# Kernel tuning notes

Measured on AMD Instinct MI355X. Metric: run time of the kernel, lower is better.

The kernel has to match this reference:

```python
import jax, jax.numpy as jnp
import numpy as np


def setup_inputs() -> dict:
    key = jax.random.key(0)
    k1, k2, k3 = jax.random.split(key, 3)
    N, E, D = 10000, 160000, 512
    x = jax.random.normal(k1, (N, D), dtype=jnp.float32)
    edge_index = jax.random.randint(k2, (2, E), 0, N, dtype=jnp.int64)
    W = jax.random.normal(k3, (D, D), dtype=jnp.float32) * (1.0 / np.sqrt(D))
    b = jnp.zeros((D,), dtype=jnp.float32)
    return {"x": x, "edge_index": edge_index, "W": W, "b": b}


def reference(x, edge_index, W, b):
    # PyG GCNConv: add self-loops, symmetric deg^-1/2 normalization,
    # linear transform (no bias in lin), scatter-add aggregate, then + bias.
    N = x.shape[0]
    loop = jnp.arange(N, dtype=edge_index.dtype)
    src = jnp.concatenate([edge_index[0], loop])  # message sources (j)
    dst = jnp.concatenate([edge_index[1], loop])  # message targets (i)
    deg = jax.ops.segment_sum(jnp.ones(src.shape, dtype=x.dtype), dst, num_segments=N)
    deg_inv_sqrt = jnp.where(deg > 0, jax.lax.rsqrt(deg), 0.0)
    norm = deg_inv_sqrt[src] * deg_inv_sqrt[dst]  # [E+N]
    h = x @ W  # [N, D] linear transform
    msg = h[src] * norm[:, None]  # gather + scale, [E+N, D]
    out = jax.ops.segment_sum(msg, dst, num_segments=N) + b
    return out
```

## Files before the change

### kernel.cpp

```cpp
#include <hip/hip_runtime.h>
#include <stdint.h>


#define D_DIM 512
#define SLOTS 64

typedef _Float16 half8 __attribute__((ext_vector_type(8)));
typedef float floatx4 __attribute__((ext_vector_type(4)));

__global__ __launch_bounds__(256) void fused_pre_kernel(const float* __restrict__ x,
                                                        const float* __restrict__ W,
                                                        const int* __restrict__ src,
                                                        const int* __restrict__ dst,
                                                        _Float16* __restrict__ Ah,
                                                        _Float16* __restrict__ Bt,
                                                        int* __restrict__ cursor,
                                                        int* __restrict__ csr,
                                                        int total8, int nxb, int E) {
    __shared__ float tile[32][33];
    int bid = blockIdx.x;
    if (bid < nxb) {
        int i = bid * 256 + threadIdx.x;
        if (i < total8) {
            const float4* p = (const float4*)x + (size_t)i * 2;
            float4 a = p[0], bq = p[1];
            half8 h;
            h[0] = (_Float16)a.x;  h[1] = (_Float16)a.y;  h[2] = (_Float16)a.z;  h[3] = (_Float16)a.w;
            h[4] = (_Float16)bq.x; h[5] = (_Float16)bq.y; h[6] = (_Float16)bq.z; h[7] = (_Float16)bq.w;
            *((half8*)Ah + i) = h;
        }
        return;
    }
    if (bid < nxb + 256) {
        int wt = bid - nxb;
        int k0 = (wt & 15) * 32, n0 = (wt >> 4) * 32;
        int tx = threadIdx.x & 31, ty = threadIdx.x >> 5;
        #pragma unroll
        for (int r = ty; r < 32; r += 8)
            tile[r][tx] = W[(size_t)(k0 + r) * D_DIM + n0 + tx];
        __syncthreads();
        #pragma unroll
        for (int r = ty; r < 32; r += 8)
            Bt[(size_t)(n0 + r) * D_DIM + k0 + tx] = (_Float16)tile[tx][r];
        return;
    }
    int e = (bid - nxb - 256) * 256 + threadIdx.x;
    if (e < E) {
        int d = dst[e];
        int pos = atomicAdd(&cursor[d], 1);
        if (pos < SLOTS) csr[(d << 6) + pos] = src[e];
    }
}

#define GBM 128
#define GBN 128
#define GBK 32
#define LDK 40

__global__ __launch_bounds__(256) void gemm_kernel(const _Float16* __restrict__ A,
                                                   const _Float16* __restrict__ Bt,
                                                   const int* __restrict__ cursor,
                                                   _Float16* __restrict__ pre,
                                                   int M, int ngb) {
    __shared__ _Float16 Asl[2][GBM * LDK];
    __shared__ _Float16 Bsl[2][GBN * LDK];

    int tid  = threadIdx.x;
    int lane = tid & 63;
    int wave = tid >> 6;
    int wr = wave >> 1, wc = wave & 1;

    int rowbase = (blockIdx.x % ngb) * GBM;
    int colbase = (blockIdx.x / ngb) * GBN;

    int s_r = tid >> 2;
    int s_k = (tid & 3) << 3;

    int fm = lane & 15;
    int fk = (lane >> 4) << 3;

    int ar0 = rowbase + s_r;      if (ar0 >= M) ar0 = M - 1;
    int ar1 = rowbase + s_r + 64; if (ar1 >= M) ar1 = M - 1;
    const _Float16* pa0 = A  + (size_t)ar0 * D_DIM + s_k;
    const _Float16* pa1 = A  + (size_t)ar1 * D_DIM + s_k;
    const _Float16* pb0 = Bt + (size_t)(colbase + s_r) * D_DIM + s_k;
    const _Float16* pb1 = Bt + (size_t)(colbase + s_r + 64) * D_DIM + s_k;

    floatx4 acc[4][4];
    #pragma unroll
    for (int i = 0; i < 4; ++i)
        #pragma unroll
        for (int j = 0; j < 4; ++j)
            #pragma unroll
            for (int e = 0; e < 4; ++e)
                acc[i][j][e] = 0.f;

    half8 av0 = *(const half8*)pa0;
    half8 av1 = *(const half8*)pa1;
    half8 bv0 = *(const half8*)pb0;
    half8 bv1 = *(const half8*)pb1;
    *(half8*)(&Asl[0][s_r * LDK + s_k])        = av0;
    *(half8*)(&Asl[0][(s_r + 64) * LDK + s_k]) = av1;
    *(half8*)(&Bsl[0][s_r * LDK + s_k])        = bv0;
    *(half8*)(&Bsl[0][(s_r + 64) * LDK + s_k]) = bv1;

    const int KT = D_DIM / GBK;
    for (int kt = 0; kt < KT; ++kt) {
        int buf = kt & 1;
        __syncthreads();

        if (kt + 1 < KT) {
            int ko = (kt + 1) * GBK;
            av0 = *(const half8*)(pa0 + ko);
            av1 = *(const half8*)(pa1 + ko);
            bv0 = *(const half8*)(pb0 + ko);
            bv1 = *(const half8*)(pb1 + ko);
        }

        half8 afrag[4], bfrag[4];
        #pragma unroll
        for (int t = 0; t < 4; ++t) {
            afrag[t] = *(const half8*)(&Asl[buf][(wr * 64 + t * 16 + fm) * LDK + fk]);
            bfrag[t] = *(const half8*)(&Bsl[buf][(wc * 64 + t * 16 + fm) * LDK + fk]);
        }
        #pragma unroll
        for (int i = 0; i < 4; ++i)
            #pragma unroll
            for (int j = 0; j < 4; ++j)
                acc[i][j] = __builtin_amdgcn_mfma_f32_16x16x32_f16(afrag[i], bfrag[j], acc[i][j], 0, 0, 0);

        if (kt + 1 < KT) {
            int nb = buf ^ 1;
            *(half8*)(&Asl[nb][s_r * LDK + s_k])        = av0;
            *(half8*)(&Asl[nb][(s_r + 64) * LDK + s_k]) = av1;
            *(half8*)(&Bsl[nb][s_r * LDK + s_k])        = bv0;
            *(half8*)(&Bsl[nb][(s_r + 64) * LDK + s_k]) = bv1;
        }
    }

    int mrow0 = (lane >> 4) << 2;
    #pragma unroll
    for (int i = 0; i < 4; ++i) {
        #pragma unroll
        for (int r = 0; r < 4; ++r) {
            int row = rowbase + wr * 64 + i * 16 + mrow0 + r;
            if (row < M) {
                float sc = rsqrtf((float)cursor[row] + 1.0f);
                #pragma unroll
                for (int j = 0; j < 4; ++j) {
                    int col = colbase + wc * 64 + j * 16 + fm;
                    pre[(size_t)row * D_DIM + col] = (_Float16)(acc[i][j][r] * sc);
                }
            }
        }
    }
}

__global__ __launch_bounds__(256) void gather_kernel(const _Float16* __restrict__ pre,
                                                     const int* __restrict__ csr,
                                                     const int* __restrict__ cursor,
                                                     const float* __restrict__ b,
                                                     float* __restrict__ out, int N) {
    int wave = threadIdx.x >> 6;
    int lane = threadIdx.x & 63;
    int node = blockIdx.x * 4 + wave;
    if (node >= N) return;
    int c8 = lane << 3;

    int cnt = cursor[node];
    int end = cnt < SLOTS ? cnt : SLOTS;
    float di = rsqrtf((float)cnt + 1.0f);
    const int* lst = csr + (node << 6);

    float acc[8];
    {
        half8 self = *(const half8*)(pre + (size_t)node * D_DIM + c8);
        #pragma unroll
        for (int e = 0; e < 8; ++e) acc[e] = (float)self[e];
    }

    int j = 0;
    for (; j + 3 < end; j += 4) {
        int s0 = lst[j];
        int s1 = lst[j + 1];
        int s2 = lst[j + 2];
        int s3 = lst[j + 3];
        half8 v0 = *(const half8*)(pre + (size_t)s0 * D_DIM + c8);
        half8 v1 = *(const half8*)(pre + (size_t)s1 * D_DIM + c8);
        half8 v2 = *(const half8*)(pre + (size_t)s2 * D_DIM + c8);
        half8 v3 = *(const half8*)(pre + (size_t)s3 * D_DIM + c8);
        #pragma unroll
        for (int e = 0; e < 8; ++e)
            acc[e] += (float)v0[e] + (float)v1[e] + (float)v2[e] + (float)v3[e];
    }
    for (; j < end; ++j) {
        int s0 = lst[j];
        half8 v0 = *(const half8*)(pre + (size_t)s0 * D_DIM + c8);
        #pragma unroll
        for (int e = 0; e < 8; ++e) acc[e] += (float)v0[e];
    }

    float4 b0 = *(const float4*)(b + c8);
    float4 b1 = *(const float4*)(b + c8 + 4);
    floatx4 o0, o1;
    o0[0] = b0.x + di * acc[0];
    o0[1] = b0.y + di * acc[1];
    o0[2] = b0.z + di * acc[2];
    o0[3] = b0.w + di * acc[3];
    o1[0] = b1.x + di * acc[4];
    o1[1] = b1.y + di * acc[5];
    o1[2] = b1.z + di * acc[6];
    o1[3] = b1.w + di * acc[7];
    __builtin_nontemporal_store(o0, (floatx4*)(out + (size_t)node * D_DIM + c8));
    __builtin_nontemporal_store(o1, (floatx4*)(out + (size_t)node * D_DIM + c8 + 4));
}

extern "C" void kernel_launch(void* const* d_in, const int* in_sizes, int n_in,
                              void* d_out, int out_size, void* d_ws, size_t ws_size,
                              hipStream_t stream) {
    const float* x  = (const float*)d_in[0];
    const int*   ei = (const int*)d_in[1];
    const float* W  = (const float*)d_in[2];
    const float* b  = (const float*)d_in[3];
    float* out = (float*)d_out;

    int N = in_sizes[0] / D_DIM;
    int E = in_sizes[1] / 2;
    const int* src = ei;
    const int* dst = ei + E;

    char* ws = (char*)d_ws;
    size_t prebytes = (size_t)N * D_DIM * sizeof(_Float16);
    size_t ahbytes  = (size_t)N * D_DIM * sizeof(_Float16);
    size_t btbytes  = (size_t)D_DIM * D_DIM * sizeof(_Float16);
    int Npad = (N + 256) & ~255;
    _Float16* pre  = (_Float16*)ws;
    _Float16* Ah   = (_Float16*)(ws + prebytes);
    _Float16* Bt   = (_Float16*)(ws + prebytes + ahbytes);
    int*      cursor = (int*)(ws + prebytes + ahbytes + btbytes);
    int*      csr    = cursor + Npad;

    (void)hipMemsetAsync(cursor, 0, (size_t)N * sizeof(int), stream);

    int total8 = (N * D_DIM) / 8;
    int nxb = (total8 + 255) / 256;
    int degb = (E + 255) / 256;
    fused_pre_kernel<<<nxb + 256 + degb, 256, 0, stream>>>(x, W, src, dst, Ah, Bt,
                                                           cursor, csr, total8, nxb, E);

    int ngb = (N + GBM - 1) / GBM;
    gemm_kernel<<<ngb * (D_DIM / GBN), 256, 0, stream>>>(Ah, Bt, cursor, pre, N, ngb);

    gather_kernel<<<(N + 3) / 4, 256, 0, stream>>>(pre, csr, cursor, b, out, N);
}
```

Baseline: 131.0 us.

## Fuse x fp32-to-fp16 conversion into GEMM A-tile loads; unroll gather by 8

The separate pass that converted x to fp16 in the pre-kernel is removed. The GEMM now reads fp32 x directly and converts it to fp16 in registers before storing to LDS. This drops the write and re-read of a 10 MB fp16 copy of x, but each GEMM block now reads twice as many bytes per A tile and x is re-read by four column blocks. The gather kernel also gains an 8-way unrolled neighbor loop to put more loads in flight.

```diff
diff --git a/kernel.cpp b/kernel.cpp
--- a/kernel.cpp
+++ b/kernel.cpp
@@ -8,32 +8,17 @@
 typedef _Float16 half8 __attribute__((ext_vector_type(8)));
 typedef float floatx4 __attribute__((ext_vector_type(4)));
 
-__global__ __launch_bounds__(256) void fused_pre_kernel(const float* __restrict__ x,
-                                                        const float* __restrict__ W,
+__global__ __launch_bounds__(256) void fused_pre_kernel(const float* __restrict__ W,
                                                         const int* __restrict__ src,
                                                         const int* __restrict__ dst,
-                                                        _Float16* __restrict__ Ah,
                                                         _Float16* __restrict__ Bt,
                                                         int* __restrict__ cursor,
                                                         int* __restrict__ csr,
-                                                        int total8, int nxb, int E) {
+                                                        int E) {
     __shared__ float tile[32][33];
     int bid = blockIdx.x;
-    if (bid < nxb) {
-        int i = bid * 256 + threadIdx.x;
-        if (i < total8) {
-            const float4* p = (const float4*)x + (size_t)i * 2;
-            float4 a = p[0], bq = p[1];
-            half8 h;
-            h[0] = (_Float16)a.x;  h[1] = (_Float16)a.y;  h[2] = (_Float16)a.z;  h[3] = (_Float16)a.w;
-            h[4] = (_Float16)bq.x; h[5] = (_Float16)bq.y; h[6] = (_Float16)bq.z; h[7] = (_Float16)bq.w;
-            *((half8*)Ah + i) = h;
-        }
-        return;
-    }
-    if (bid < nxb + 256) {
-        int wt = bid - nxb;
-        int k0 = (wt & 15) * 32, n0 = (wt >> 4) * 32;
+    if (bid < 256) {
+        int k0 = (bid & 15) * 32, n0 = (bid >> 4) * 32;
         int tx = threadIdx.x & 31, ty = threadIdx.x >> 5;
         #pragma unroll
         for (int r = ty; r < 32; r += 8)
@@ -44,7 +29,7 @@
             Bt[(size_t)(n0 + r) * D_DIM + k0 + tx] = (_Float16)tile[tx][r];
         return;
     }
-    int e = (bid - nxb - 256) * 256 + threadIdx.x;
+    int e = (bid - 256) * 256 + threadIdx.x;
     if (e < E) {
         int d = dst[e];
         int pos = atomicAdd(&cursor[d], 1);
@@ -57,7 +42,7 @@
 #define GBK 32
 #define LDK 40
 
-__global__ __launch_bounds__(256) void gemm_kernel(const _Float16* __restrict__ A,
+__global__ __launch_bounds__(256) void gemm_kernel(const float* __restrict__ X,
                                                    const _Float16* __restrict__ Bt,
                                                    const int* __restrict__ cursor,
                                                    _Float16* __restrict__ pre,
@@ -81,8 +66,8 @@
 
     int ar0 = rowbase + s_r;      if (ar0 >= M) ar0 = M - 1;
     int ar1 = rowbase + s_r + 64; if (ar1 >= M) ar1 = M - 1;
-    const _Float16* pa0 = A  + (size_t)ar0 * D_DIM + s_k;
-    const _Float16* pa1 = A  + (size_t)ar1 * D_DIM + s_k;
+    const float* px0 = X + (size_t)ar0 * D_DIM + s_k;
+    const float* px1 = X + (size_t)ar1 * D_DIM + s_k;
     const _Float16* pb0 = Bt + (size_t)(colbase + s_r) * D_DIM + s_k;
     const _Float16* pb1 = Bt + (size_t)(colbase + s_r + 64) * D_DIM + s_k;
 
@@ -95,10 +80,15 @@
             for (int e = 0; e < 4; ++e)
                 acc[i][j][e] = 0.f;
 
-    half8 av0 = *(const half8*)pa0;
-    half8 av1 = *(const half8*)pa1;
+    float4 xa0 = *(const float4*)px0,       xb0 = *(const float4*)(px0 + 4);
+    float4 xa1 = *(const float4*)px1,       xb1 = *(const float4*)(px1 + 4);
     half8 bv0 = *(const half8*)pb0;
     half8 bv1 = *(const half8*)pb1;
+    half8 av0, av1;
+    av0[0] = (_Float16)xa0.x; av0[1] = (_Float16)xa0.y; av0[2] = (_Float16)xa0.z; av0[3] = (_Float16)xa0.w;
+    av0[4] = (_Float16)xb0.x; av0[5] = (_Float16)xb0.y; av0[6] = (_Float16)xb0.z; av0[7] = (_Float16)xb0.w;
+    av1[0] = (_Float16)xa1.x; av1[1] = (_Float16)xa1.y; av1[2] = (_Float16)xa1.z; av1[3] = (_Float16)xa1.w;
+    av1[4] = (_Float16)xb1.x; av1[5] = (_Float16)xb1.y; av1[6] = (_Float16)xb1.z; av1[7] = (_Float16)xb1.w;
     *(half8*)(&Asl[0][s_r * LDK + s_k])        = av0;
     *(half8*)(&Asl[0][(s_r + 64) * LDK + s_k]) = av1;
     *(half8*)(&Bsl[0][s_r * LDK + s_k])        = bv0;
@@ -111,8 +101,8 @@
 
         if (kt + 1 < KT) {
             int ko = (kt + 1) * GBK;
-            av0 = *(const half8*)(pa0 + ko);
-            av1 = *(const half8*)(pa1 + ko);
+            xa0 = *(const float4*)(px0 + ko); xb0 = *(const float4*)(px0 + ko + 4);
+            xa1 = *(const float4*)(px1 + ko); xb1 = *(const float4*)(px1 + ko + 4);
             bv0 = *(const half8*)(pb0 + ko);
             bv1 = *(const half8*)(pb1 + ko);
         }
@@ -131,6 +121,10 @@
 
         if (kt + 1 < KT) {
             int nb = buf ^ 1;
+            av0[0] = (_Float16)xa0.x; av0[1] = (_Float16)xa0.y; av0[2] = (_Float16)xa0.z; av0[3] = (_Float16)xa0.w;
+            av0[4] = (_Float16)xb0.x; av0[5] = (_Float16)xb0.y; av0[6] = (_Float16)xb0.z; av0[7] = (_Float16)xb0.w;
+            av1[0] = (_Float16)xa1.x; av1[1] = (_Float16)xa1.y; av1[2] = (_Float16)xa1.z; av1[3] = (_Float16)xa1.w;
+            av1[4] = (_Float16)xb1.x; av1[5] = (_Float16)xb1.y; av1[6] = (_Float16)xb1.z; av1[7] = (_Float16)xb1.w;
             *(half8*)(&Asl[nb][s_r * LDK + s_k])        = av0;
             *(half8*)(&Asl[nb][(s_r + 64) * LDK + s_k]) = av1;
             *(half8*)(&Bsl[nb][s_r * LDK + s_k])        = bv0;
@@ -180,22 +174,35 @@
     }
 
     int j = 0;
+    for (; j + 7 < end; j += 8) {
+        half8 v[8];
+        #pragma unroll
+        for (int u = 0; u < 8; ++u) {
+            int s = lst[j + u];
+            v[u] = *(const half8*)(pre + (size_t)s * D_DIM + c8);
+        }
+        #pragma unroll
+        for (int e = 0; e < 8; ++e) {
+            float t = 0.f;
+            #pragma unroll
+            for (int u = 0; u < 8; ++u) t += (float)v[u][e];
+            acc[e] += t;
+        }
+    }
     for (; j + 3 < end; j += 4) {
-        int s0 = lst[j];
-        int s1 = lst[j + 1];
-        int s2 = lst[j + 2];
-        int s3 = lst[j + 3];
-        half8 v0 = *(const half8*)(pre + (size_t)s0 * D_DIM + c8);
-        half8 v1 = *(const half8*)(pre + (size_t)s1 * D_DIM + c8);
-        half8 v2 = *(const half8*)(pre + (size_t)s2 * D_DIM + c8);
-        half8 v3 = *(const half8*)(pre + (size_t)s3 * D_DIM + c8);
+        half8 v[4];
+        #pragma unroll
+        for (int u = 0; u < 4; ++u) {
+            int s = lst[j + u];
+            v[u] = *(const half8*)(pre + (size_t)s * D_DIM + c8);
+        }
         #pragma unroll
         for (int e = 0; e < 8; ++e)
-            acc[e] += (float)v0[e] + (float)v1[e] + (float)v2[e] + (float)v3[e];
+            acc[e] += (float)v[0][e] + (float)v[1][e] + (float)v[2][e] + (float)v[3][e];
     }
     for (; j < end; ++j) {
-        int s0 = lst[j];
-        half8 v0 = *(const half8*)(pre + (size_t)s0 * D_DIM + c8);
+        int s = lst[j];
+        half8 v0 = *(const half8*)(pre + (size_t)s * D_DIM + c8);
         #pragma unroll
         for (int e = 0; e < 8; ++e) acc[e] += (float)v0[e];
     }
@@ -231,25 +238,20 @@
 
     char* ws = (char*)d_ws;
     size_t prebytes = (size_t)N * D_DIM * sizeof(_Float16);
-    size_t ahbytes  = (size_t)N * D_DIM * sizeof(_Float16);
     size_t btbytes  = (size_t)D_DIM * D_DIM * sizeof(_Float16);
     int Npad = (N + 256) & ~255;
     _Float16* pre  = (_Float16*)ws;
-    _Float16* Ah   = (_Float16*)(ws + prebytes);
-    _Float16* Bt   = (_Float16*)(ws + prebytes + ahbytes);
-    int*      cursor = (int*)(ws + prebytes + ahbytes + btbytes);
+    _Float16* Bt   = (_Float16*)(ws + prebytes);
+    int*      cursor = (int*)(ws + prebytes + btbytes);
     int*      csr    = cursor + Npad;
 
     (void)hipMemsetAsync(cursor, 0, (size_t)N * sizeof(int), stream);
 
-    int total8 = (N * D_DIM) / 8;
-    int nxb = (total8 + 255) / 256;
     int degb = (E + 255) / 256;
-    fused_pre_kernel<<<nxb + 256 + degb, 256, 0, stream>>>(x, W, src, dst, Ah, Bt,
-                                                           cursor, csr, total8, nxb, E);
+    fused_pre_kernel<<<256 + degb, 256, 0, stream>>>(W, src, dst, Bt, cursor, csr, E);
 
     int ngb = (N + GBM - 1) / GBM;
-    gemm_kernel<<<ngb * (D_DIM / GBN), 256, 0, stream>>>(Ah, Bt, cursor, pre, N, ngb);
+    gemm_kernel<<<ngb * (D_DIM / GBN), 256, 0, stream>>>(x, Bt, cursor, pre, N, ngb);
 
     gather_kernel<<<(N + 3) / 4, 256, 0, stream>>>(pre, csr, cursor, b, out, N);
 }
```

After: 129.4 us. No clear change (-1.2%).
